# Kernel tuning notes

Measured on AMD Instinct MI355X. Metric: run time of the kernel, lower is better.

The kernel has to match this reference:

```python
import jax, jax.numpy as jnp
import numpy as np

B, N, FN, FE = 8, 256, 64, 64  # batch, nodes, node feat, edge feat


def gnn_layer(A, x, e, We, be, Wn, bn):
    # A: [B,N,N] float mask, x: [B,N,Fn], e: [B,N,N,Fe_in]
    b, n, fn = x.shape
    xi = jnp.broadcast_to(x[:, :, None, :], (b, n, n, fn))  # sender feats
    xj = jnp.broadcast_to(x[:, None, :, :], (b, n, n, fn))  # receiver feats
    h = jnp.concatenate([xi, xj, e], axis=-1)               # [B,N,N,2Fn+Fe]
    e_new = jax.nn.relu(jnp.einsum('bijk,kf->bijf', h, We) + be) * A[..., None]
    deg = jnp.clip(jnp.sum(A, axis=2), 1.0, None)           # [B,N]
    agg = jnp.sum(e_new, axis=2) / deg[..., None]           # mean over neighbors
    x_new = jax.nn.relu(jnp.concatenate([x, agg], axis=-1) @ Wn + bn)
    return x_new, e_new


def setup_inputs() -> dict:
    key = jax.random.key(0)
    ks = jax.random.split(key, 20)
    s = 0.05
    inp = {
        'edge_index': jax.random.randint(ks[0], (B, N, N), 0, 2, dtype=jnp.int32),
        'x': jax.random.normal(ks[1], (B, N, FN), dtype=jnp.float32),
        'edge_attr': jax.random.normal(ks[2], (B, N, N, FE), dtype=jnp.float32),
    }
    # 3 GNN layers: edge-update MLP (2Fn+Fe -> Fe) and node-update (Fn+Fe -> Fn)
    for l in range(3):
        inp[f'We{l}'] = jax.random.normal(ks[3 + 4 * l], (2 * FN + FE, FE), jnp.float32) * s
        inp[f'be{l}'] = jnp.zeros((FE,), jnp.float32)
        inp[f'Wn{l}'] = jax.random.normal(ks[4 + 4 * l], (FN + FE, FN), jnp.float32) * s
        inp[f'bn{l}'] = jnp.zeros((FN,), jnp.float32)
    # spectral-norm MLP head: Fe -> Fe -> Fe -> 1
    inp['W1'] = jax.random.normal(ks[15], (FE, FE), jnp.float32) * s
    inp['b1'] = jnp.zeros((FE,), jnp.float32)
    inp['W2'] = jax.random.normal(ks[16], (FE, FE), jnp.float32) * s
    inp['b2'] = jnp.zeros((FE,), jnp.float32)
    inp['W3'] = jax.random.normal(ks[17], (FE, 1), jnp.float32) * s
    inp['b3'] = jnp.zeros((1,), jnp.float32)
    return inp


def reference(edge_index, x, edge_attr,
              We0, be0, Wn0, bn0,
              We1, be1, Wn1, bn1,
              We2, be2, Wn2, bn2,
              W1, b1, W2, b2, W3, b3):
    A = edge_index.astype(jnp.float32)
    x = x.astype(jnp.float32)
    # layer 0 updates both nodes and edges
    x1, e = gnn_layer(A, x, edge_attr, We0, be0, Wn0, bn0)
    # middle layer(s): node output discarded (as in original forward)
    _, e = gnn_layer(A, x1, e, We1, be1, Wn1, bn1)
    # last layer
    _, edges = gnn_layer(A, x1, e, We2, be2, Wn2, bn2)
    # end == 'edge_mean'
    v = jnp.mean(edges, axis=(1, 2))  # [B, FE]
    h = jax.nn.relu(v @ W1 + b1)
    h = jax.nn.relu(h @ W2 + b2)
    out = h @ W3 + b3                  # [B, 1]
    return jnp.squeeze(out, axis=-1)   # [B]
```

## Files before the change

### kernel.cpp

```cpp
#include <hip/hip_runtime.h>

#define BB 8
#define NN 256
#define FF 64

typedef float f32x4 __attribute__((ext_vector_type(4)));
typedef short s16x8 __attribute__((ext_vector_type(8)));
typedef unsigned short u16;

#define MFMA_BF16(a, b, c) __builtin_amdgcn_mfma_f32_16x16x32_bf16(a, b, c, 0, 0, 0)

__device__ inline u16 f2bf(float x) {
    unsigned u = __float_as_uint(x);
    u += 0x7FFFu + ((u >> 16) & 1u);
    return (u16)(u >> 16);
}
__device__ inline float bf2f(u16 h) { return __uint_as_float(((unsigned)h) << 16); }

__device__ inline s16x8 cvt_a(float4 v0, float4 v1) {
    s16x8 a;
    a[0] = (short)f2bf(v0.x); a[1] = (short)f2bf(v0.y);
    a[2] = (short)f2bf(v0.z); a[3] = (short)f2bf(v0.w);
    a[4] = (short)f2bf(v1.x); a[5] = (short)f2bf(v1.y);
    a[6] = (short)f2bf(v1.z); a[7] = (short)f2bf(v1.w);
    return a;
}

__global__ __launch_bounds__(256) void wprep_kernel(
    const float* __restrict__ We0, const float* __restrict__ We1,
    const float* __restrict__ We2, u16* __restrict__ wimg)
{
    const float* src =
        (blockIdx.x == 0 ? We0 : (blockIdx.x == 1 ? We1 : We2)) + 2 * FF * FF;
    u16* hi = wimg + blockIdx.x * 8192;
    u16* lo = hi + 4096;
    for (int idx = threadIdx.x; idx < 4096; idx += 256) {
        const int f = idx >> 6, rem = idx & 63, cs = rem >> 3, j = rem & 7;
        const int k = ((cs ^ (f & 7)) << 3) | j;
        const float wv = src[k * FF + f];
        const u16 h = f2bf(wv);
        hi[idx] = h;
        lo[idx] = f2bf(wv - bf2f(h));
    }
}

__global__ __launch_bounds__(256) void pq_kernel(
    const float* __restrict__ x, const float* __restrict__ We,
    const float* __restrict__ be, float* __restrict__ P, float* __restrict__ Q,
    float* __restrict__ agg)
{
    const int rl = threadIdx.x >> 6, f = threadIdx.x & 63;
    const int r = blockIdx.x * 4 + rl;
    __shared__ float xs[4][FF];
    xs[rl][f] = x[r * FF + f];
    agg[r * FF + f] = 0.f;
    __syncthreads();
    float p = be[f], q = 0.f;
#pragma unroll
    for (int k = 0; k < FF; ++k) {
        const float xv = xs[rl][k];
        p = fmaf(xv, We[k * FF + f], p);
        q = fmaf(xv, We[(FF + k) * FF + f], q);
    }
    P[r * FF + f] = p;
    Q[r * FF + f] = q;
}

__global__ __launch_bounds__(256) void edge0_kernel(
    const float* __restrict__ e_in, const u16* __restrict__ whi,
    const u16* __restrict__ wlo, const float* __restrict__ P,
    const float* __restrict__ Q, const int* __restrict__ A,
    float* __restrict__ e_out, float* __restrict__ agg)
{
    __shared__ u16 Whl[4096], Wll[4096];
    __shared__ float Al[128], Pl[64];

    const int tid = threadIdx.x;
    const int bt  = blockIdx.x;
    const int bi  = bt >> 1;
    const int b   = bi >> 8;
    const int j0  = (bt & 1) << 7;

#pragma unroll
    for (int m = 0; m < 2; ++m) {
        ((uint4*)Whl)[tid + 256 * m] = ((const uint4*)whi)[tid + 256 * m];
        ((uint4*)Wll)[tid + 256 * m] = ((const uint4*)wlo)[tid + 256 * m];
    }
    if (tid < 128) Al[tid] = (float)A[bi * NN + j0 + tid];
    if (tid < 64)  Pl[tid] = P[bi * FF + tid];

    const int w = tid >> 6, lane = tid & 63;
    const int quad = lane >> 4, l15 = lane & 15, l7 = lane & 7;
    const int e_base = 32 * w;

    const float* erow = e_in + ((size_t)bi * NN + j0) * FF;

    s16x8 afr[2][2];
#pragma unroll
    for (int ks = 0; ks < 2; ++ks)
#pragma unroll
        for (int et = 0; et < 2; ++et) {
            const float* p = erow + (e_base + et * 16 + l15) * FF + ks * 32 + quad * 8;
            afr[ks][et] = cvt_a(*(const float4*)p, *(const float4*)(p + 4));
        }

    float qv[2][4][4];
    const float* Qb = Q + (size_t)b * NN * FF;
#pragma unroll
    for (int et = 0; et < 2; ++et)
#pragma unroll
        for (int ft = 0; ft < 4; ++ft)
#pragma unroll
            for (int r = 0; r < 4; ++r)
                qv[et][ft][r] =
                    Qb[(j0 + e_base + et * 16 + quad * 4 + r) * FF + ft * 16 + l15];

    __syncthreads();

    f32x4 acc[2][4];
#pragma unroll
    for (int et = 0; et < 2; ++et)
#pragma unroll
        for (int ft = 0; ft < 4; ++ft) acc[et][ft] = (f32x4){0.f, 0.f, 0.f, 0.f};

#pragma unroll
    for (int ks = 0; ks < 2; ++ks)
#pragma unroll
        for (int ft = 0; ft < 4; ++ft) {
            const int f  = ft * 16 + l15;
            const int ca = (ks * 4 + quad) ^ l7;
            const s16x8 bh = *(const s16x8*)&Whl[f * 64 + ca * 8];
            const s16x8 bl = *(const s16x8*)&Wll[f * 64 + ca * 8];
#pragma unroll
            for (int et = 0; et < 2; ++et) {
                acc[et][ft] = MFMA_BF16(afr[ks][et], bh, acc[et][ft]);
                acc[et][ft] = MFMA_BF16(afr[ks][et], bl, acc[et][ft]);
            }
        }

    float psum[4] = {0.f, 0.f, 0.f, 0.f};
#pragma unroll
    for (int et = 0; et < 2; ++et)
#pragma unroll
        for (int ft = 0; ft < 4; ++ft)
#pragma unroll
            for (int r = 0; r < 4; ++r) {
                const int el = e_base + et * 16 + quad * 4 + r;
                const int f  = ft * 16 + l15;
                const float val = acc[et][ft][r] + Pl[f] + qv[et][ft][r];
                const float rv  = fmaxf(val, 0.f) * Al[el];
                e_out[((size_t)bi * NN + j0 + el) * FF + f] = rv;
                psum[ft] += rv;
            }
#pragma unroll
    for (int ft = 0; ft < 4; ++ft) {
        psum[ft] += __shfl_down(psum[ft], 32);
        psum[ft] += __shfl_down(psum[ft], 16);
    }
    if (lane < 16) {
#pragma unroll
        for (int ft = 0; ft < 4; ++ft)
            atomicAdd(&agg[bi * FF + ft * 16 + l15], psum[ft]);
    }
}

__global__ __launch_bounds__(256) void nodepq_kernel(
    const float* __restrict__ x, const float* __restrict__ agg,
    const int* __restrict__ A,
    const float* __restrict__ Wn, const float* __restrict__ bn,
    const float* __restrict__ We1, const float* __restrict__ be1,
    const float* __restrict__ We2, const float* __restrict__ be2,
    float* __restrict__ P1, float* __restrict__ Q1,
    float* __restrict__ P2, float* __restrict__ Q2, float* __restrict__ v)
{
    const int rl = threadIdx.x >> 6, f = threadIdx.x & 63;
    const int r = blockIdx.x * 4 + rl;
    __shared__ float s[4][2 * FF];
    __shared__ float x1s[4][FF];

    float da = (float)A[r * NN + f] + (float)A[r * NN + f + 64] +
               (float)A[r * NN + f + 128] + (float)A[r * NN + f + 192];
#pragma unroll
    for (int off = 32; off > 0; off >>= 1) da += __shfl_down(da, off, 64);
    const float deg = fmaxf(__shfl(da, 0, 64), 1.0f);

    s[rl][f]      = x[r * FF + f];
    s[rl][FF + f] = agg[r * FF + f] / deg;
    if (blockIdx.x == 0) {
        v[threadIdx.x] = 0.f;
        v[256 + threadIdx.x] = 0.f;
    }
    __syncthreads();
    float a = bn[f];
#pragma unroll
    for (int k = 0; k < 2 * FF; ++k) a = fmaf(s[rl][k], Wn[k * FF + f], a);
    x1s[rl][f] = fmaxf(a, 0.f);
    __syncthreads();
    float p1 = be1[f], q1 = 0.f, p2 = be2[f], q2 = 0.f;
#pragma unroll
    for (int k = 0; k < FF; ++k) {
        const float xv = x1s[rl][k];
        p1 = fmaf(xv, We1[k * FF + f], p1);
        q1 = fmaf(xv, We1[(FF + k) * FF + f], q1);
        p2 = fmaf(xv, We2[k * FF + f], p2);
        q2 = fmaf(xv, We2[(FF + k) * FF + f], q2);
    }
    P1[r * FF + f] = p1;  Q1[r * FF + f] = q1;
    P2[r * FF + f] = p2;  Q2[r * FF + f] = q2;
}

__global__ __launch_bounds__(256) void edge12_kernel(
    const float* __restrict__ e_in,
    const u16* __restrict__ w1hi, const u16* __restrict__ w1lo,
    const u16* __restrict__ w2hi, const u16* __restrict__ w2lo,
    const float* __restrict__ P1, const float* __restrict__ Q1,
    const float* __restrict__ P2, const float* __restrict__ Q2,
    const int* __restrict__ A, float* __restrict__ v)
{
    __shared__ u16 W1h[4096], W1l[4096], W2h[4096], W2l[4096];
    __shared__ u16 E2[128 * 64];
    __shared__ float Al[128], Pl1[64], Pl2[64], red[64];

    const int tid = threadIdx.x;
    const int bt  = blockIdx.x;
    const int bi  = bt >> 1;
    const int b   = bi >> 8;
    const int j0  = (bt & 1) << 7;

#pragma unroll
    for (int m = 0; m < 2; ++m) {
        ((uint4*)W1h)[tid + 256 * m] = ((const uint4*)w1hi)[tid + 256 * m];
        ((uint4*)W1l)[tid + 256 * m] = ((const uint4*)w1lo)[tid + 256 * m];
        ((uint4*)W2h)[tid + 256 * m] = ((const uint4*)w2hi)[tid + 256 * m];
        ((uint4*)W2l)[tid + 256 * m] = ((const uint4*)w2lo)[tid + 256 * m];
    }
    if (tid < 128) Al[tid] = (float)A[bi * NN + j0 + tid];
    if (tid < 64) {
        Pl1[tid] = P1[bi * FF + tid];
        Pl2[tid] = P2[bi * FF + tid];
        red[tid] = 0.f;
    }

    const int w = tid >> 6, lane = tid & 63;
    const int quad = lane >> 4, l15 = lane & 15, l7 = lane & 7;
    const int e_base = 32 * w;

    const float* erow = e_in + ((size_t)bi * NN + j0) * FF;

    s16x8 afr[2][2];
#pragma unroll
    for (int ks = 0; ks < 2; ++ks)
#pragma unroll
        for (int et = 0; et < 2; ++et) {
            const float* p = erow + (e_base + et * 16 + l15) * FF + ks * 32 + quad * 8;
            afr[ks][et] = cvt_a(*(const float4*)p, *(const float4*)(p + 4));
        }

    float qv[2][4][4];
    {
        const float* Q1b = Q1 + (size_t)b * NN * FF;
#pragma unroll
        for (int et = 0; et < 2; ++et)
#pragma unroll
            for (int ft = 0; ft < 4; ++ft)
#pragma unroll
                for (int r = 0; r < 4; ++r)
                    qv[et][ft][r] =
                        Q1b[(j0 + e_base + et * 16 + quad * 4 + r) * FF + ft * 16 + l15];
    }

    __syncthreads();

    f32x4 acc[2][4];
#pragma unroll
    for (int et = 0; et < 2; ++et)
#pragma unroll
        for (int ft = 0; ft < 4; ++ft) acc[et][ft] = (f32x4){0.f, 0.f, 0.f, 0.f};

#pragma unroll
    for (int ks = 0; ks < 2; ++ks)
#pragma unroll
        for (int ft = 0; ft < 4; ++ft) {
            const int f  = ft * 16 + l15;
            const int ca = (ks * 4 + quad) ^ l7;
            const s16x8 bh = *(const s16x8*)&W1h[f * 64 + ca * 8];
            const s16x8 bl = *(const s16x8*)&W1l[f * 64 + ca * 8];
#pragma unroll
            for (int et = 0; et < 2; ++et) {
                acc[et][ft] = MFMA_BF16(afr[ks][et], bh, acc[et][ft]);
                acc[et][ft] = MFMA_BF16(afr[ks][et], bl, acc[et][ft]);
            }
        }

#pragma unroll
    for (int et = 0; et < 2; ++et)
#pragma unroll
        for (int ft = 0; ft < 4; ++ft)
#pragma unroll
            for (int r = 0; r < 4; ++r) {
                const int el = e_base + et * 16 + quad * 4 + r;
                const int f  = ft * 16 + l15;
                const float val = acc[et][ft][r] + Pl1[f] + qv[et][ft][r];
                const float rv  = fmaxf(val, 0.f) * Al[el];
                const int c  = f >> 3;
                const int cs = c ^ (el & 7);
                E2[el * 64 + cs * 8 + l7] = f2bf(rv);
            }

    {
        const float* Q2b = Q2 + (size_t)b * NN * FF;
#pragma unroll
        for (int et = 0; et < 2; ++et)
#pragma unroll
            for (int ft = 0; ft < 4; ++ft)
#pragma unroll
                for (int r = 0; r < 4; ++r)
                    qv[et][ft][r] =
                        Q2b[(j0 + e_base + et * 16 + quad * 4 + r) * FF + ft * 16 + l15];
    }

    __syncthreads();

#pragma unroll
    for (int et = 0; et < 2; ++et)
#pragma unroll
        for (int ft = 0; ft < 4; ++ft) acc[et][ft] = (f32x4){0.f, 0.f, 0.f, 0.f};

#pragma unroll
    for (int ks = 0; ks < 2; ++ks) {
        s16x8 a2[2];
#pragma unroll
        for (int et = 0; et < 2; ++et) {
            const int e  = e_base + et * 16 + l15;
            const int ca = (ks * 4 + quad) ^ l7;
            a2[et] = *(const s16x8*)&E2[e * 64 + ca * 8];
        }
#pragma unroll
        for (int ft = 0; ft < 4; ++ft) {
            const int f  = ft * 16 + l15;
            const int ca = (ks * 4 + quad) ^ l7;
            const s16x8 bh = *(const s16x8*)&W2h[f * 64 + ca * 8];
            const s16x8 bl = *(const s16x8*)&W2l[f * 64 + ca * 8];
#pragma unroll
            for (int et = 0; et < 2; ++et) {
                acc[et][ft] = MFMA_BF16(a2[et], bh, acc[et][ft]);
                acc[et][ft] = MFMA_BF16(a2[et], bl, acc[et][ft]);
            }
        }
    }

    float psum[4] = {0.f, 0.f, 0.f, 0.f};
#pragma unroll
    for (int et = 0; et < 2; ++et)
#pragma unroll
        for (int ft = 0; ft < 4; ++ft)
#pragma unroll
            for (int r = 0; r < 4; ++r) {
                const int el = e_base + et * 16 + quad * 4 + r;
                const int f  = ft * 16 + l15;
                const float val = acc[et][ft][r] + Pl2[f] + qv[et][ft][r];
                psum[ft] += fmaxf(val, 0.f) * Al[el];
            }
#pragma unroll
    for (int ft = 0; ft < 4; ++ft) {
        psum[ft] += __shfl_down(psum[ft], 32);
        psum[ft] += __shfl_down(psum[ft], 16);
    }
    if (lane < 16) {
#pragma unroll
        for (int ft = 0; ft < 4; ++ft)
            atomicAdd(&red[ft * 16 + l15], psum[ft]);
    }
    __syncthreads();
    if (tid < 64) atomicAdd(&v[b * FF + tid], red[tid]);
}

__global__ __launch_bounds__(64) void head_kernel(
    const float* __restrict__ vsum, const float* __restrict__ W1,
    const float* __restrict__ b1, const float* __restrict__ W2,
    const float* __restrict__ b2, const float* __restrict__ W3,
    const float* __restrict__ b3, float* __restrict__ out)
{
    const int f = threadIdx.x;
    __shared__ float hv[BB][FF];
    __shared__ float h1[BB][FF];
#pragma unroll
    for (int b = 0; b < BB; ++b) hv[b][f] = vsum[b * FF + f] * (1.0f / 65536.0f);
    __syncthreads();
#pragma unroll
    for (int b = 0; b < BB; ++b) {
        float acc = b1[f];
#pragma unroll
        for (int k = 0; k < FF; ++k) acc = fmaf(hv[b][k], W1[k * FF + f], acc);
        h1[b][f] = fmaxf(acc, 0.f);
    }
    __syncthreads();
#pragma unroll
    for (int b = 0; b < BB; ++b) {
        float acc = b2[f];
#pragma unroll
        for (int k = 0; k < FF; ++k) acc = fmaf(h1[b][k], W2[k * FF + f], acc);
        hv[b][f] = fmaxf(acc, 0.f);
    }
    __syncthreads();
#pragma unroll
    for (int b = 0; b < BB; ++b) {
        float p = hv[b][f] * W3[f];
#pragma unroll
        for (int off = 32; off > 0; off >>= 1) p += __shfl_down(p, off);
        if (f == 0) out[b] = p + b3[0];
    }
}

extern "C" void kernel_launch(void* const* d_in, const int* in_sizes, int n_in,
                              void* d_out, int out_size, void* d_ws, size_t ws_size,
                              hipStream_t stream)
{
    const int*   A      = (const int*)d_in[0];
    const float* x      = (const float*)d_in[1];
    float*       e_attr = (float*)d_in[2];

    const float* We0 = (const float*)d_in[3];
    const float* be0 = (const float*)d_in[4];
    const float* Wn0 = (const float*)d_in[5];
    const float* bn0 = (const float*)d_in[6];
    const float* We1 = (const float*)d_in[7];
    const float* be1 = (const float*)d_in[8];
    const float* We2 = (const float*)d_in[11];
    const float* be2 = (const float*)d_in[12];
    const float* W1 = (const float*)d_in[15];
    const float* b1 = (const float*)d_in[16];
    const float* W2 = (const float*)d_in[17];
    const float* b2 = (const float*)d_in[18];
    const float* W3 = (const float*)d_in[19];
    const float* b3 = (const float*)d_in[20];
    float* out = (float*)d_out;
    (void)in_sizes; (void)n_in; (void)out_size; (void)ws_size;

    const int R = BB * NN;
    float* P1  = (float*)d_ws;
    float* Q1  = P1 + R * FF;
    float* P2  = Q1 + R * FF;
    float* Q2  = P2 + R * FF;
    float* agg = Q2 + R * FF;
    float* v   = agg + R * FF;
    u16*  wimg = (u16*)(v + 512);

    const int EB = 2 * R;

    wprep_kernel<<<3, 256, 0, stream>>>(We0, We1, We2, wimg);
    pq_kernel<<<R / 4, 256, 0, stream>>>(x, We0, be0, P1, Q1, agg);
    edge0_kernel<<<EB, 256, 0, stream>>>(e_attr, wimg, wimg + 4096, P1, Q1, A,
                                         e_attr, agg);
    nodepq_kernel<<<R / 4, 256, 0, stream>>>(x, agg, A, Wn0, bn0, We1, be1,
                                             We2, be2, P1, Q1, P2, Q2, v);
    edge12_kernel<<<EB, 256, 0, stream>>>(e_attr,
                                          wimg + 8192, wimg + 12288,
                                          wimg + 16384, wimg + 20480,
                                          P1, Q1, P2, Q2, A, v);
    head_kernel<<<1, 64, 0, stream>>>(v, W1, b1, W2, b2, W3, b3, out);
}
```

Before: 360.0 us.

## Store intermediate edge features as bf16 and share LDS weight buffers

edge0 now writes its output edge tensor as bf16 in a per-block tile layout, overwriting the input buffer in place. edge12 reads that bf16 tile directly as MFMA A-fragments and skips the fp32-to-bf16 conversion. This halves the intermediate edge traffic, which dominates this memory-bound pipeline. edge12 also reuses one pair of LDS weight buffers for both layers, staging the layer-2 weights in registers, and both kernels get a launch bound of 4 blocks per SM to raise occupancy. The cost is an extra barrier. The in-place overwrite is only safe if each block reads its own input region before writing, which the per-block tile indexing appears to preserve.

```diff
diff --git a/kernel.cpp b/kernel.cpp
--- a/kernel.cpp
+++ b/kernel.cpp
@@ -66,11 +66,11 @@
     Q[r * FF + f] = q;
 }
 
-__global__ __launch_bounds__(256) void edge0_kernel(
-    const float* __restrict__ e_in, const u16* __restrict__ whi,
+__global__ __launch_bounds__(256, 4) void edge0_kernel(
+    const float* e_in, const u16* __restrict__ whi,
     const u16* __restrict__ wlo, const float* __restrict__ P,
     const float* __restrict__ Q, const int* __restrict__ A,
-    float* __restrict__ e_out, float* __restrict__ agg)
+    u16* e1_out, float* __restrict__ agg)
 {
     __shared__ u16 Whl[4096], Wll[4096];
     __shared__ float Al[128], Pl[64];
@@ -138,6 +138,7 @@
             }
         }
 
+    u16* dst = e1_out + (size_t)bt * 16384;
     float psum[4] = {0.f, 0.f, 0.f, 0.f};
 #pragma unroll
     for (int et = 0; et < 2; ++et)
@@ -149,7 +150,7 @@
                 const int f  = ft * 16 + l15;
                 const float val = acc[et][ft][r] + Pl[f] + qv[et][ft][r];
                 const float rv  = fmaxf(val, 0.f) * Al[el];
-                e_out[((size_t)bi * NN + j0 + el) * FF + f] = rv;
+                dst[el * 64 + f] = f2bf(rv);
                 psum[ft] += rv;
             }
 #pragma unroll
@@ -209,15 +210,15 @@
     P2[r * FF + f] = p2;  Q2[r * FF + f] = q2;
 }
 
-__global__ __launch_bounds__(256) void edge12_kernel(
-    const float* __restrict__ e_in,
+__global__ __launch_bounds__(256, 4) void edge12_kernel(
+    const u16* __restrict__ e1,
     const u16* __restrict__ w1hi, const u16* __restrict__ w1lo,
     const u16* __restrict__ w2hi, const u16* __restrict__ w2lo,
     const float* __restrict__ P1, const float* __restrict__ Q1,
     const float* __restrict__ P2, const float* __restrict__ Q2,
     const int* __restrict__ A, float* __restrict__ v)
 {
-    __shared__ u16 W1h[4096], W1l[4096], W2h[4096], W2l[4096];
+    __shared__ u16 Wh[4096], Wl[4096];
     __shared__ u16 E2[128 * 64];
     __shared__ float Al[128], Pl1[64], Pl2[64], red[64];
 
@@ -227,12 +228,15 @@
     const int b   = bi >> 8;
     const int j0  = (bt & 1) << 7;
 
+    const uint4 w2h0 = ((const uint4*)w2hi)[tid];
+    const uint4 w2h1 = ((const uint4*)w2hi)[tid + 256];
+    const uint4 w2l0 = ((const uint4*)w2lo)[tid];
+    const uint4 w2l1 = ((const uint4*)w2lo)[tid + 256];
+
 #pragma unroll
     for (int m = 0; m < 2; ++m) {
-        ((uint4*)W1h)[tid + 256 * m] = ((const uint4*)w1hi)[tid + 256 * m];
-        ((uint4*)W1l)[tid + 256 * m] = ((const uint4*)w1lo)[tid + 256 * m];
-        ((uint4*)W2h)[tid + 256 * m] = ((const uint4*)w2hi)[tid + 256 * m];
-        ((uint4*)W2l)[tid + 256 * m] = ((const uint4*)w2lo)[tid + 256 * m];
+        ((uint4*)Wh)[tid + 256 * m] = ((const uint4*)w1hi)[tid + 256 * m];
+        ((uint4*)Wl)[tid + 256 * m] = ((const uint4*)w1lo)[tid + 256 * m];
     }
     if (tid < 128) Al[tid] = (float)A[bi * NN + j0 + tid];
     if (tid < 64) {
@@ -245,16 +249,14 @@
     const int quad = lane >> 4, l15 = lane & 15, l7 = lane & 7;
     const int e_base = 32 * w;
 
-    const float* erow = e_in + ((size_t)bi * NN + j0) * FF;
-
+    const u16* etile = e1 + (size_t)bt * 16384;
     s16x8 afr[2][2];
 #pragma unroll
     for (int ks = 0; ks < 2; ++ks)
 #pragma unroll
-        for (int et = 0; et < 2; ++et) {
-            const float* p = erow + (e_base + et * 16 + l15) * FF + ks * 32 + quad * 8;
-            afr[ks][et] = cvt_a(*(const float4*)p, *(const float4*)(p + 4));
-        }
+        for (int et = 0; et < 2; ++et)
+            afr[ks][et] = *(const s16x8*)
+                &etile[(e_base + et * 16 + l15) * 64 + ks * 32 + quad * 8];
 
     float qv[2][4][4];
     {
@@ -283,8 +285,8 @@
         for (int ft = 0; ft < 4; ++ft) {
             const int f  = ft * 16 + l15;
             const int ca = (ks * 4 + quad) ^ l7;
-            const s16x8 bh = *(const s16x8*)&W1h[f * 64 + ca * 8];
-            const s16x8 bl = *(const s16x8*)&W1l[f * 64 + ca * 8];
+            const s16x8 bh = *(const s16x8*)&Wh[f * 64 + ca * 8];
+            const s16x8 bl = *(const s16x8*)&Wl[f * 64 + ca * 8];
 #pragma unroll
             for (int et = 0; et < 2; ++et) {
                 acc[et][ft] = MFMA_BF16(afr[ks][et], bh, acc[et][ft]);
@@ -321,6 +323,13 @@
 
     __syncthreads();
 
+    ((uint4*)Wh)[tid]       = w2h0;
+    ((uint4*)Wh)[tid + 256] = w2h1;
+    ((uint4*)Wl)[tid]       = w2l0;
+    ((uint4*)Wl)[tid + 256] = w2l1;
+
+    __syncthreads();
+
 #pragma unroll
     for (int et = 0; et < 2; ++et)
 #pragma unroll
@@ -339,8 +348,8 @@
         for (int ft = 0; ft < 4; ++ft) {
             const int f  = ft * 16 + l15;
             const int ca = (ks * 4 + quad) ^ l7;
-            const s16x8 bh = *(const s16x8*)&W2h[f * 64 + ca * 8];
-            const s16x8 bl = *(const s16x8*)&W2l[f * 64 + ca * 8];
+            const s16x8 bh = *(const s16x8*)&Wh[f * 64 + ca * 8];
+            const s16x8 bl = *(const s16x8*)&Wl[f * 64 + ca * 8];
 #pragma unroll
             for (int et = 0; et < 2; ++et) {
                 acc[et][ft] = MFMA_BF16(a2[et], bh, acc[et][ft]);
@@ -451,10 +460,10 @@
     wprep_kernel<<<3, 256, 0, stream>>>(We0, We1, We2, wimg);
     pq_kernel<<<R / 4, 256, 0, stream>>>(x, We0, be0, P1, Q1, agg);
     edge0_kernel<<<EB, 256, 0, stream>>>(e_attr, wimg, wimg + 4096, P1, Q1, A,
-                                         e_attr, agg);
+                                         (u16*)e_attr, agg);
     nodepq_kernel<<<R / 4, 256, 0, stream>>>(x, agg, A, Wn0, bn0, We1, be1,
                                              We2, be2, P1, Q1, P2, Q2, v);
-    edge12_kernel<<<EB, 256, 0, stream>>>(e_attr,
+    edge12_kernel<<<EB, 256, 0, stream>>>((const u16*)e_attr,
                                           wimg + 8192, wimg + 12288,
                                           wimg + 16384, wimg + 20480,
                                           P1, Q1, P2, Q2, A, v);
```

Measured after the change: 365.5 us. About the same (+1.5%).

## Recompute layer-0 edges in fused edge kernel instead of storing them

Applied to the files above, without the earlier changes.

Layer 0's edge kernel no longer writes the full edge tensor to global memory; it only accumulates the neighbor aggregate. The later edge kernel re-reads the original edge attributes and recomputes layer 0's edge output in LDS before running layers 1 and 2. This trades a full fp32 edge-tensor write plus read for one extra small MFMA GEMM per tile. Weight buffers in LDS are reused across the three layers, with the next layer's weights prefetched into registers, and occupancy hints are added. The input buffer is also no longer overwritten.

```diff
diff --git a/kernel.cpp b/kernel.cpp
--- a/kernel.cpp
+++ b/kernel.cpp
@@ -66,11 +66,11 @@
     Q[r * FF + f] = q;
 }
 
-__global__ __launch_bounds__(256) void edge0_kernel(
+__global__ __launch_bounds__(256, 4) void edge0_kernel(
     const float* __restrict__ e_in, const u16* __restrict__ whi,
     const u16* __restrict__ wlo, const float* __restrict__ P,
     const float* __restrict__ Q, const int* __restrict__ A,
-    float* __restrict__ e_out, float* __restrict__ agg)
+    float* __restrict__ agg)
 {
     __shared__ u16 Whl[4096], Wll[4096];
     __shared__ float Al[128], Pl[64];
@@ -148,9 +148,7 @@
                 const int el = e_base + et * 16 + quad * 4 + r;
                 const int f  = ft * 16 + l15;
                 const float val = acc[et][ft][r] + Pl[f] + qv[et][ft][r];
-                const float rv  = fmaxf(val, 0.f) * Al[el];
-                e_out[((size_t)bi * NN + j0 + el) * FF + f] = rv;
-                psum[ft] += rv;
+                psum[ft] += fmaxf(val, 0.f) * Al[el];
             }
 #pragma unroll
     for (int ft = 0; ft < 4; ++ft) {
@@ -209,17 +207,19 @@
     P2[r * FF + f] = p2;  Q2[r * FF + f] = q2;
 }
 
-__global__ __launch_bounds__(256) void edge12_kernel(
+__global__ __launch_bounds__(256, 4) void edge123_kernel(
     const float* __restrict__ e_in,
+    const u16* __restrict__ w0hi, const u16* __restrict__ w0lo,
     const u16* __restrict__ w1hi, const u16* __restrict__ w1lo,
     const u16* __restrict__ w2hi, const u16* __restrict__ w2lo,
+    const float* __restrict__ P0, const float* __restrict__ Q0,
     const float* __restrict__ P1, const float* __restrict__ Q1,
     const float* __restrict__ P2, const float* __restrict__ Q2,
     const int* __restrict__ A, float* __restrict__ v)
 {
-    __shared__ u16 W1h[4096], W1l[4096], W2h[4096], W2l[4096];
-    __shared__ u16 E2[128 * 64];
-    __shared__ float Al[128], Pl1[64], Pl2[64], red[64];
+    __shared__ u16 Wh[4096], Wl[4096];
+    __shared__ u16 E[128 * 64];
+    __shared__ float Al[128], Pl0[64], Pl1[64], Pl2[64], red[64];
 
     const int tid = threadIdx.x;
     const int bt  = blockIdx.x;
@@ -227,15 +227,19 @@
     const int b   = bi >> 8;
     const int j0  = (bt & 1) << 7;
 
+    uint4 sh0 = ((const uint4*)w1hi)[tid];
+    uint4 sh1 = ((const uint4*)w1hi)[tid + 256];
+    uint4 sl0 = ((const uint4*)w1lo)[tid];
+    uint4 sl1 = ((const uint4*)w1lo)[tid + 256];
+
 #pragma unroll
     for (int m = 0; m < 2; ++m) {
-        ((uint4*)W1h)[tid + 256 * m] = ((const uint4*)w1hi)[tid + 256 * m];
-        ((uint4*)W1l)[tid + 256 * m] = ((const uint4*)w1lo)[tid + 256 * m];
-        ((uint4*)W2h)[tid + 256 * m] = ((const uint4*)w2hi)[tid + 256 * m];
-        ((uint4*)W2l)[tid + 256 * m] = ((const uint4*)w2lo)[tid + 256 * m];
+        ((uint4*)Wh)[tid + 256 * m] = ((const uint4*)w0hi)[tid + 256 * m];
+        ((uint4*)Wl)[tid + 256 * m] = ((const uint4*)w0lo)[tid + 256 * m];
     }
     if (tid < 128) Al[tid] = (float)A[bi * NN + j0 + tid];
     if (tid < 64) {
+        Pl0[tid] = P0[bi * FF + tid];
         Pl1[tid] = P1[bi * FF + tid];
         Pl2[tid] = P2[bi * FF + tid];
         red[tid] = 0.f;
@@ -246,7 +250,6 @@
     const int e_base = 32 * w;
 
     const float* erow = e_in + ((size_t)bi * NN + j0) * FF;
-
     s16x8 afr[2][2];
 #pragma unroll
     for (int ks = 0; ks < 2; ++ks)
@@ -258,7 +261,7 @@
 
     float qv[2][4][4];
     {
-        const float* Q1b = Q1 + (size_t)b * NN * FF;
+        const float* Qb = Q0 + (size_t)b * NN * FF;
 #pragma unroll
         for (int et = 0; et < 2; ++et)
 #pragma unroll
@@ -266,7 +269,7 @@
 #pragma unroll
                 for (int r = 0; r < 4; ++r)
                     qv[et][ft][r] =
-                        Q1b[(j0 + e_base + et * 16 + quad * 4 + r) * FF + ft * 16 + l15];
+                        Qb[(j0 + e_base + et * 16 + quad * 4 + r) * FF + ft * 16 + l15];
     }
 
     __syncthreads();
@@ -283,14 +286,82 @@
         for (int ft = 0; ft < 4; ++ft) {
             const int f  = ft * 16 + l15;
             const int ca = (ks * 4 + quad) ^ l7;
-            const s16x8 bh = *(const s16x8*)&W1h[f * 64 + ca * 8];
-            const s16x8 bl = *(const s16x8*)&W1l[f * 64 + ca * 8];
+            const s16x8 bh = *(const s16x8*)&Wh[f * 64 + ca * 8];
+            const s16x8 bl = *(const s16x8*)&Wl[f * 64 + ca * 8];
 #pragma unroll
             for (int et = 0; et < 2; ++et) {
                 acc[et][ft] = MFMA_BF16(afr[ks][et], bh, acc[et][ft]);
                 acc[et][ft] = MFMA_BF16(afr[ks][et], bl, acc[et][ft]);
             }
         }
+
+#pragma unroll
+    for (int et = 0; et < 2; ++et)
+#pragma unroll
+        for (int ft = 0; ft < 4; ++ft)
+#pragma unroll
+            for (int r = 0; r < 4; ++r) {
+                const int el = e_base + et * 16 + quad * 4 + r;
+                const int f  = ft * 16 + l15;
+                const float val = acc[et][ft][r] + Pl0[f] + qv[et][ft][r];
+                const float rv  = fmaxf(val, 0.f) * Al[el];
+                const int c  = f >> 3;
+                const int cs = c ^ (el & 7);
+                E[el * 64 + cs * 8 + l7] = f2bf(rv);
+            }
+
+    {
+        const float* Qb = Q1 + (size_t)b * NN * FF;
+#pragma unroll
+        for (int et = 0; et < 2; ++et)
+#pragma unroll
+            for (int ft = 0; ft < 4; ++ft)
+#pragma unroll
+                for (int r = 0; r < 4; ++r)
+                    qv[et][ft][r] =
+                        Qb[(j0 + e_base + et * 16 + quad * 4 + r) * FF + ft * 16 + l15];
+    }
+
+    __syncthreads();
+
+    ((uint4*)Wh)[tid]       = sh0;
+    ((uint4*)Wh)[tid + 256] = sh1;
+    ((uint4*)Wl)[tid]       = sl0;
+    ((uint4*)Wl)[tid + 256] = sl1;
+    sh0 = ((const uint4*)w2hi)[tid];
+    sh1 = ((const uint4*)w2hi)[tid + 256];
+    sl0 = ((const uint4*)w2lo)[tid];
+    sl1 = ((const uint4*)w2lo)[tid + 256];
+
+    __syncthreads();
+
+#pragma unroll
+    for (int et = 0; et < 2; ++et)
+#pragma unroll
+        for (int ft = 0; ft < 4; ++ft) acc[et][ft] = (f32x4){0.f, 0.f, 0.f, 0.f};
+
+#pragma unroll
+    for (int ks = 0; ks < 2; ++ks) {
+        s16x8 a2[2];
+#pragma unroll
+        for (int et = 0; et < 2; ++et) {
+            const int e  = e_base + et * 16 + l15;
+            const int ca = (ks * 4 + quad) ^ l7;
+            a2[et] = *(const s16x8*)&E[e * 64 + ca * 8];
+        }
+#pragma unroll
+        for (int ft = 0; ft < 4; ++ft) {
+            const int f  = ft * 16 + l15;
+            const int ca = (ks * 4 + quad) ^ l7;
+            const s16x8 bh = *(const s16x8*)&Wh[f * 64 + ca * 8];
+            const s16x8 bl = *(const s16x8*)&Wl[f * 64 + ca * 8];
+#pragma unroll
+            for (int et = 0; et < 2; ++et) {
+                acc[et][ft] = MFMA_BF16(a2[et], bh, acc[et][ft]);
+                acc[et][ft] = MFMA_BF16(a2[et], bl, acc[et][ft]);
+            }
+        }
+    }
 
 #pragma unroll
     for (int et = 0; et < 2; ++et)
@@ -304,11 +375,11 @@
                 const float rv  = fmaxf(val, 0.f) * Al[el];
                 const int c  = f >> 3;
                 const int cs = c ^ (el & 7);
-                E2[el * 64 + cs * 8 + l7] = f2bf(rv);
+                E[el * 64 + cs * 8 + l7] = f2bf(rv);
             }
 
     {
-        const float* Q2b = Q2 + (size_t)b * NN * FF;
+        const float* Qb = Q2 + (size_t)b * NN * FF;
 #pragma unroll
         for (int et = 0; et < 2; ++et)
 #pragma unroll
@@ -316,8 +387,15 @@
 #pragma unroll
                 for (int r = 0; r < 4; ++r)
                     qv[et][ft][r] =
-                        Q2b[(j0 + e_base + et * 16 + quad * 4 + r) * FF + ft * 16 + l15];
-    }
+                        Qb[(j0 + e_base + et * 16 + quad * 4 + r) * FF + ft * 16 + l15];
+    }
+
+    __syncthreads();
+
+    ((uint4*)Wh)[tid]       = sh0;
+    ((uint4*)Wh)[tid + 256] = sh1;
+    ((uint4*)Wl)[tid]       = sl0;
+    ((uint4*)Wl)[tid + 256] = sl1;
 
     __syncthreads();
 
@@ -333,14 +411,14 @@
         for (int et = 0; et < 2; ++et) {
             const int e  = e_base + et * 16 + l15;
             const int ca = (ks * 4 + quad) ^ l7;
-            a2[et] = *(const s16x8*)&E2[e * 64 + ca * 8];
+            a2[et] = *(const s16x8*)&E[e * 64 + ca * 8];
         }
 #pragma unroll
         for (int ft = 0; ft < 4; ++ft) {
             const int f  = ft * 16 + l15;
             const int ca = (ks * 4 + quad) ^ l7;
-            const s16x8 bh = *(const s16x8*)&W2h[f * 64 + ca * 8];
-            const s16x8 bl = *(const s16x8*)&W2l[f * 64 + ca * 8];
+            const s16x8 bh = *(const s16x8*)&Wh[f * 64 + ca * 8];
+            const s16x8 bl = *(const s16x8*)&Wl[f * 64 + ca * 8];
 #pragma unroll
             for (int et = 0; et < 2; ++et) {
                 acc[et][ft] = MFMA_BF16(a2[et], bh, acc[et][ft]);
@@ -418,7 +496,7 @@
 {
     const int*   A      = (const int*)d_in[0];
     const float* x      = (const float*)d_in[1];
-    float*       e_attr = (float*)d_in[2];
+    const float* e_attr = (const float*)d_in[2];
 
     const float* We0 = (const float*)d_in[3];
     const float* be0 = (const float*)d_in[4];
@@ -438,7 +516,9 @@
     (void)in_sizes; (void)n_in; (void)out_size; (void)ws_size;
 
     const int R = BB * NN;
-    float* P1  = (float*)d_ws;
+    float* P0  = (float*)d_ws;
+    float* Q0  = P0 + R * FF;
+    float* P1  = Q0 + R * FF;
     float* Q1  = P1 + R * FF;
     float* P2  = Q1 + R * FF;
     float* Q2  = P2 + R * FF;
@@ -449,14 +529,15 @@
     const int EB = 2 * R;
 
     wprep_kernel<<<3, 256, 0, stream>>>(We0, We1, We2, wimg);
-    pq_kernel<<<R / 4, 256, 0, stream>>>(x, We0, be0, P1, Q1, agg);
-    edge0_kernel<<<EB, 256, 0, stream>>>(e_attr, wimg, wimg + 4096, P1, Q1, A,
-                                         e_attr, agg);
+    pq_kernel<<<R / 4, 256, 0, stream>>>(x, We0, be0, P0, Q0, agg);
+    edge0_kernel<<<EB, 256, 0, stream>>>(e_attr, wimg, wimg + 4096, P0, Q0, A,
+                                         agg);
     nodepq_kernel<<<R / 4, 256, 0, stream>>>(x, agg, A, Wn0, bn0, We1, be1,
                                              We2, be2, P1, Q1, P2, Q2, v);
-    edge12_kernel<<<EB, 256, 0, stream>>>(e_attr,
-                                          wimg + 8192, wimg + 12288,
-                                          wimg + 16384, wimg + 20480,
-                                          P1, Q1, P2, Q2, A, v);
+    edge123_kernel<<<EB, 256, 0, stream>>>(e_attr,
+                                           wimg,         wimg + 4096,
+                                           wimg + 8192,  wimg + 12288,
+                                           wimg + 16384, wimg + 20480,
+                                           P0, Q0, P1, Q1, P2, Q2, A, v);
     head_kernel<<<1, 64, 0, stream>>>(v, W1, b1, W2, b2, W3, b3, out);
 }
```

New measurement: 406.5 us. 12.9% more time.
